# Kernel tuning notes

Measured on AMD Instinct MI355X. Metric: run time of the kernel, lower is better.

The kernel has to match this reference:

```python
import jax, jax.numpy as jnp
import numpy as np

DIM = 2048
H = 16
DK = 128
DV = 128
KCONV = 4
EPS = 1e-6
B = 2
S = 2048
KD = H * DK  # 2048
VD = H * DV  # 2048


def setup_inputs() -> dict:
    key = jax.random.key(0)
    ks = jax.random.split(key, 16)
    sc = 0.02
    inp = {
        "x": jax.random.normal(ks[0], (B, S, DIM), dtype=jnp.float32),
        "Wq": jax.random.normal(ks[1], (KD, DIM), dtype=jnp.float32) * sc,
        "Wk": jax.random.normal(ks[2], (KD, DIM), dtype=jnp.float32) * sc,
        "Wv": jax.random.normal(ks[3], (VD, DIM), dtype=jnp.float32) * sc,
        "Wa": jax.random.normal(ks[4], (H, DIM), dtype=jnp.float32) * sc,
        "Wb": jax.random.normal(ks[5], (H, DIM), dtype=jnp.float32) * sc,
        "Wg": jax.random.normal(ks[6], (VD, DIM), dtype=jnp.float32) * sc,
        "Wo": jax.random.normal(ks[7], (DIM, VD), dtype=jnp.float32) * sc,
        "cw_q": jax.random.normal(ks[8], (KD, KCONV), dtype=jnp.float32) * 0.3,
        "cb_q": jnp.zeros((KD,), dtype=jnp.float32),
        "cw_k": jax.random.normal(ks[9], (KD, KCONV), dtype=jnp.float32) * 0.3,
        "cb_k": jnp.zeros((KD,), dtype=jnp.float32),
        "cw_v": jax.random.normal(ks[10], (VD, KCONV), dtype=jnp.float32) * 0.3,
        "cb_v": jnp.zeros((VD,), dtype=jnp.float32),
        "A_log": jnp.zeros((H,), dtype=jnp.float32),
        "dt_bias": jnp.zeros((H,), dtype=jnp.float32),
        "norm_w": jnp.ones((VD,), dtype=jnp.float32),
    }
    return inp


def _causal_conv(x, w, b):
    # x: [B, S, C]; w: [C, K]; b: [C]. Depthwise causal conv (zero init state) + SiLU.
    Bb, Ss, C = x.shape
    xp = jnp.pad(x, ((0, 0), (KCONV - 1, 0), (0, 0)))
    out = b
    for j in range(KCONV):
        out = out + xp[:, j:j + Ss, :] * w[:, j]
    return jax.nn.silu(out)


def _l2norm(x):
    n = jnp.sqrt(jnp.sum(x * x, axis=-1, keepdims=True))
    return x / jnp.maximum(n, 1e-12)


def _forward(x, Wq, Wk, Wv, Wa, Wb, Wg, Wo, cw_q, cb_q, cw_k, cb_k, cw_v, cb_v,
             A_log, dt_bias, norm_w):
    Bb, Ss, _ = x.shape
    q = _causal_conv(x @ Wq.T, cw_q, cb_q)  # [B,S,KD]
    k = _causal_conv(x @ Wk.T, cw_k, cb_k)
    v = _causal_conv(x @ Wv.T, cw_v, cb_v)

    a = x @ Wa.T  # [B,S,H]
    b = x @ Wb.T
    g = jnp.exp(-jnp.exp(A_log)[None, None, :] * jax.nn.softplus(a + dt_bias[None, None, :]))
    beta = jax.nn.sigmoid(b)

    q = _l2norm(q.reshape(Bb, Ss, H, DK))
    k = _l2norm(k.reshape(Bb, Ss, H, DK))
    v = v.reshape(Bb, Ss, H, DV)

    S0 = jnp.zeros((Bb, H, DK, DV), dtype=x.dtype)

    def step(Sstate, inputs):
        q_t, k_t, v_t, g_t, beta_t = inputs  # [B,H,DK],[B,H,DK],[B,H,DV],[B,H],[B,H]
        retrieved = jnp.einsum('bhkv,bhk->bhv', Sstate, k_t)
        error = v_t - g_t[..., None] * retrieved
        update = k_t[..., :, None] * (beta_t[..., None] * error)[..., None, :]
        Snew = g_t[..., None, None] * Sstate + update
        o_t = jnp.einsum('bhkv,bhk->bhv', Snew, q_t)
        return Snew, o_t

    # scan over time: move time axis to front
    xs = (q.transpose(1, 0, 2, 3), k.transpose(1, 0, 2, 3), v.transpose(1, 0, 2, 3),
          g.transpose(1, 0, 2), beta.transpose(1, 0, 2))
    _, o = jax.lax.scan(step, S0, xs)  # o: [S,B,H,DV]
    o = o.transpose(1, 0, 2, 3).reshape(Bb, Ss, VD)

    # RMSNorm
    o = o * jax.lax.rsqrt(jnp.mean(o * o, axis=-1, keepdims=True) + EPS) * norm_w
    o = o * jax.nn.silu(x @ Wg.T)
    return o @ Wo.T


def reference(x, Wq, Wk, Wv, Wa, Wb, Wg, Wo, cw_q, cb_q, cw_k, cb_k, cw_v, cb_v,
              A_log, dt_bias, norm_w):
    return _forward(x, Wq, Wk, Wv, Wa, Wb, Wg, Wo, cw_q, cb_q, cw_k, cb_k,
                    cw_v, cb_v, A_log, dt_bias, norm_w)
```

## Files before the change

kernel.cpp:

```cpp
#include <hip/hip_runtime.h>

#define S_LEN   2048
#define NH      16
#define DIM     2048
#define KD      2048
#define VD      2048
#define MB      1048576ull
#define CT      64
#define NC      32

typedef short  short8  __attribute__((ext_vector_type(8)));
typedef short  short4v __attribute__((ext_vector_type(4)));
typedef float  floatx4 __attribute__((ext_vector_type(4)));

#define MFMA(a, b, c) __builtin_amdgcn_mfma_f32_16x16x32_bf16((a), (b), (c), 0, 0, 0)

__device__ inline short f2bf(float x) {
    unsigned u = __float_as_uint(x);
    unsigned r = (u + 0x7fffu + ((u >> 16) & 1u)) >> 16;
    return (short)r;
}
__device__ inline float bf2f(short s) {
    return __uint_as_float(((unsigned)(unsigned short)s) << 16);
}
__device__ inline float silu_f(float x) { return x / (1.f + __expf(-x)); }

__device__ inline short8 neg8(short8 a) {
    unsigned* p = (unsigned*)&a;
    p[0] ^= 0x80008000u; p[1] ^= 0x80008000u;
    p[2] ^= 0x80008000u; p[3] ^= 0x80008000u;
    return a;
}

__device__ inline void load_lds16(const void* g, void* l) {
    __builtin_amdgcn_global_load_lds(
        (const __attribute__((address_space(1))) unsigned int*)g,
        (__attribute__((address_space(3))) unsigned int*)l, 16, 0, 0);
}

__global__ __launch_bounds__(256) void cvt_all_kernel(
    const float* __restrict__ x,  const float* __restrict__ Wq,
    const float* __restrict__ Wk, const float* __restrict__ Wv,
    const float* __restrict__ Wg, const float* __restrict__ Wo,
    short* __restrict__ xb,  short* __restrict__ Wqb, short* __restrict__ Wkb,
    short* __restrict__ Wvb, short* __restrict__ Wgb, short* __restrict__ Wob) {
    const float* in; short* out; int n8;
    switch (blockIdx.y) {
        case 0:  in = x;  out = xb;  n8 = 1048576; break;
        case 1:  in = Wq; out = Wqb; n8 = 524288;  break;
        case 2:  in = Wk; out = Wkb; n8 = 524288;  break;
        case 3:  in = Wv; out = Wvb; n8 = 524288;  break;
        case 4:  in = Wg; out = Wgb; n8 = 524288;  break;
        default: in = Wo; out = Wob; n8 = 524288;  break;
    }
    int i = blockIdx.x * 256 + threadIdx.x;
    if (i >= n8) return;
    float4 a = ((const float4*)in)[2 * i];
    float4 b = ((const float4*)in)[2 * i + 1];
    short8 o;
    o[0] = f2bf(a.x); o[1] = f2bf(a.y); o[2] = f2bf(a.z); o[3] = f2bf(a.w);
    o[4] = f2bf(b.x); o[5] = f2bf(b.y); o[6] = f2bf(b.z); o[7] = f2bf(b.w);
    ((short8*)out)[i] = o;
}

__device__ inline void store_c(float* C, size_t idx, float v) { C[idx] = v; }
__device__ inline void store_c(short* C, size_t idx, float v) { C[idx] = f2bf(v); }

template <typename OutT>
__device__ inline void gemm_tile(const short* __restrict__ A, const short* __restrict__ Bw,
                                 OutT* __restrict__ C, int mtile, int ntile) {
    __shared__ short lA[128 * 32];
    __shared__ short lB[128 * 32];
    const int K = 2048, N = 2048;
    int t    = threadIdx.x;
    int wave = t >> 6;
    int lane = t & 63;
    int m0 = mtile * 128, n0 = ntile * 128;
    int wm = (wave & 1) * 64;
    int wn = (wave >> 1) * 64;

    floatx4 acc[4][4];
#pragma unroll
    for (int i = 0; i < 4; ++i)
#pragma unroll
        for (int j = 0; j < 4; ++j) acc[i][j] = (floatx4){0.f, 0.f, 0.f, 0.f};

    int fr = lane & 15;
    int fk = (lane >> 4) * 8;

    for (int k0 = 0; k0 < K; k0 += 32) {
#pragma unroll
        for (int p = 0; p < 2; ++p) {
            int c   = p * 256 + t;
            int row = c >> 2, kp = c & 3;
            const short* ga = A  + (size_t)(m0 + row) * K + k0 + kp * 8;
            const short* gb = Bw + (size_t)(n0 + row) * K + k0 + kp * 8;
            short* la = lA + (size_t)(p * 256 + wave * 64) * 8;
            short* lb = lB + (size_t)(p * 256 + wave * 64) * 8;
            load_lds16(ga, la);
            load_lds16(gb, lb);
        }
        __syncthreads();
        short8 af[4], bfr[4];
#pragma unroll
        for (int i = 0; i < 4; ++i) af[i]  = *(const short8*)(lA + (wm + i * 16 + fr) * 32 + fk);
#pragma unroll
        for (int j = 0; j < 4; ++j) bfr[j] = *(const short8*)(lB + (wn + j * 16 + fr) * 32 + fk);
#pragma unroll
        for (int i = 0; i < 4; ++i)
#pragma unroll
            for (int j = 0; j < 4; ++j)
                acc[i][j] = MFMA(af[i], bfr[j], acc[i][j]);
        __syncthreads();
    }
    int cr = (lane >> 4) * 4;
    int cc = lane & 15;
#pragma unroll
    for (int i = 0; i < 4; ++i)
#pragma unroll
        for (int j = 0; j < 4; ++j)
#pragma unroll
            for (int r = 0; r < 4; ++r)
                store_c(C, (size_t)(m0 + wm + i * 16 + cr + r) * N + (n0 + wn + j * 16 + cc),
                        acc[i][j][r]);
}

__global__ __launch_bounds__(256) void gemm_qkvg(const short* __restrict__ A,
    const short* __restrict__ B0, const short* __restrict__ B1,
    const short* __restrict__ B2, const short* __restrict__ B3,
    short* __restrict__ C0, short* __restrict__ C1,
    short* __restrict__ C2, short* __restrict__ C3) {
    const short* Bw; short* C;
    switch (blockIdx.z) {
        case 0:  Bw = B0; C = C0; break;
        case 1:  Bw = B1; C = C1; break;
        case 2:  Bw = B2; C = C2; break;
        default: Bw = B3; C = C3; break;
    }
    gemm_tile<short>(A, Bw, C, blockIdx.x, blockIdx.y);
}

__global__ __launch_bounds__(256) void gemm_out(const short* __restrict__ A,
    const short* __restrict__ Bw, float* __restrict__ C) {
    gemm_tile<float>(A, Bw, C, blockIdx.x, blockIdx.y);
}

__global__ __launch_bounds__(256) void ab_kernel(const float* __restrict__ x,
    const float* __restrict__ Wa, const float* __restrict__ Wb,
    const float* __restrict__ Alog, const float* __restrict__ dtb,
    float* __restrict__ gdec, float* __restrict__ beta) {
    __shared__ float xs[2048];
    __shared__ float red[32][9];
    int m = blockIdx.x, t = threadIdx.x;
    const float* xr = x + (size_t)m * DIM;
    for (int i = t; i < 512; i += 256) ((float4*)xs)[i] = ((const float4*)xr)[i];
    __syncthreads();
    int col = t >> 3, part = t & 7;
    const float* wr = (col < 16) ? (Wa + (size_t)col * DIM) : (Wb + (size_t)(col - 16) * DIM);
    float s = 0.f;
    int kb = part * 256;
#pragma unroll 4
    for (int k = 0; k < 256; k += 4) {
        float4 xv = *(const float4*)(xs + kb + k);
        float4 wv = *(const float4*)(wr + kb + k);
        s += xv.x * wv.x + xv.y * wv.y + xv.z * wv.z + xv.w * wv.w;
    }
    red[col][part] = s;
    __syncthreads();
    if (t < 32) {
        float a = 0.f;
#pragma unroll
        for (int p = 0; p < 8; ++p) a += red[t][p];
        if (t < 16) {
            float sp = a + dtb[t];
            float softp = (sp > 20.f) ? sp : log1pf(expf(sp));
            gdec[(size_t)m * NH + t] = expf(-expf(Alog[t]) * softp);
        } else {
            int h = t - 16;
            beta[(size_t)m * NH + h] = 1.f / (1.f + expf(-a));
        }
    }
}

__global__ __launch_bounds__(256) void conv_kernel(
    const short* __restrict__ qr, const short* __restrict__ kr, const short* __restrict__ vr,
    const float* __restrict__ cwq, const float* __restrict__ cbq,
    const float* __restrict__ cwk, const float* __restrict__ cbk,
    const float* __restrict__ cwv, const float* __restrict__ cbv,
    short* __restrict__ qn, short* __restrict__ kn, short* __restrict__ vc) {
    int gw   = blockIdx.x * 4 + (threadIdx.x >> 6);
    int lane = threadIdx.x & 63;
    int h  = gw & (NH - 1);
    int m  = gw >> 4;
    int tt = m & (S_LEN - 1);
    int c  = h * 128 + lane * 2;
    size_t rowbase = (size_t)m * KD + c;

    float4 wq0 = ((const float4*)cwq)[c], wq1 = ((const float4*)cwq)[c + 1];
    float4 wk0 = ((const float4*)cwk)[c], wk1 = ((const float4*)cwk)[c + 1];
    float4 wv0 = ((const float4*)cwv)[c], wv1 = ((const float4*)cwv)[c + 1];
    float q0 = cbq[c], q1 = cbq[c + 1];
    float k0 = cbk[c], k1 = cbk[c + 1];
    float v0 = cbv[c], v1 = cbv[c + 1];
    const float* wq0a = (const float*)&wq0; const float* wq1a = (const float*)&wq1;
    const float* wk0a = (const float*)&wk0; const float* wk1a = (const float*)&wk1;
    const float* wv0a = (const float*)&wv0; const float* wv1a = (const float*)&wv1;
#pragma unroll
    for (int j = 0; j < 4; ++j) {
        int ts = tt - 3 + j;
        if (ts >= 0) {
            long long rb = (long long)rowbase + (long long)(j - 3) * KD;
            unsigned uq = *(const unsigned*)(qr + rb);
            unsigned uk = *(const unsigned*)(kr + rb);
            unsigned uv = *(const unsigned*)(vr + rb);
            q0 += bf2f((short)(uq & 0xffff)) * wq0a[j]; q1 += bf2f((short)(uq >> 16)) * wq1a[j];
            k0 += bf2f((short)(uk & 0xffff)) * wk0a[j]; k1 += bf2f((short)(uk >> 16)) * wk1a[j];
            v0 += bf2f((short)(uv & 0xffff)) * wv0a[j]; v1 += bf2f((short)(uv >> 16)) * wv1a[j];
        }
    }
    q0 = silu_f(q0); q1 = silu_f(q1);
    k0 = silu_f(k0); k1 = silu_f(k1);
    v0 = silu_f(v0); v1 = silu_f(v1);

    float sq = q0 * q0 + q1 * q1;
    float sk = k0 * k0 + k1 * k1;
#pragma unroll
    for (int off = 1; off < 64; off <<= 1) {
        sq += __shfl_xor(sq, off);
        sk += __shfl_xor(sk, off);
    }
    float iq = 1.f / fmaxf(sqrtf(sq), 1e-12f);
    float ik = 1.f / fmaxf(sqrtf(sk), 1e-12f);
    unsigned oq = (unsigned)(unsigned short)f2bf(q0 * iq) | ((unsigned)(unsigned short)f2bf(q1 * iq) << 16);
    unsigned ok = (unsigned)(unsigned short)f2bf(k0 * ik) | ((unsigned)(unsigned short)f2bf(k1 * ik) << 16);
    unsigned ov = (unsigned)(unsigned short)f2bf(v0)      | ((unsigned)(unsigned short)f2bf(v1)      << 16);
    *(unsigned*)(qn + rowbase) = oq;
    *(unsigned*)(kn + rowbase) = ok;
    *(unsigned*)(vc + rowbase) = ov;
}

__global__ __launch_bounds__(256) void solve_kernel(
    const short* __restrict__ kn, const short* __restrict__ vn,
    const float* __restrict__ gdec, const float* __restrict__ beta,
    short* __restrict__ UvT, short* __restrict__ Tk) {
    __shared__ short Pn[64][72];
    __shared__ short Pt[64][72];
    __shared__ short UT[128][72];
    __shared__ float Ls[64];
    __shared__ float Bs[64];

    int wg   = blockIdx.x;
    int half = wg & 1;
    int c    = (wg >> 1) & 31;
    int bh   = wg >> 6;
    int b = bh >> 4, h = bh & 15;
    int tid = threadIdx.x;
    int wave = tid >> 6, lane = tid & 63;
    int quad = lane >> 4, l16 = lane & 15;

    const short* Kb = kn + ((size_t)(b * S_LEN + c * CT)) * KD + h * 128;
    const short* Vb = vn + ((size_t)(b * S_LEN + c * CT)) * KD + h * 128;

    if (wave == 0) {
        float lg = __logf(gdec[((size_t)(b * S_LEN + c * CT) + lane) * NH + h]);
#pragma unroll
        for (int off = 1; off < 64; off <<= 1) {
            float y = __shfl_up(lg, off);
            if (lane >= off) lg += y;
        }
        Ls[lane] = lg;
        Bs[lane] = beta[((size_t)(b * S_LEN + c * CT) + lane) * NH + h];
    }
    __syncthreads();

    {
        floatx4 acc[4];
#pragma unroll
        for (int i = 0; i < 4; ++i) acc[i] = (floatx4){0.f, 0.f, 0.f, 0.f};
        for (int ks = 0; ks < 4; ++ks) {
            short8 af = *(const short8*)(Kb + (size_t)(wave * 16 + l16) * KD + ks * 32 + quad * 8);
#pragma unroll
            for (int it = 0; it < 4; ++it) {
                short8 bf = *(const short8*)(Kb + (size_t)(it * 16 + l16) * KD + ks * 32 + quad * 8);
                acc[it] = MFMA(af, bf, acc[it]);
            }
        }
#pragma unroll
        for (int it = 0; it < 4; ++it) {
            int icol = it * 16 + l16;
#pragma unroll
            for (int r = 0; r < 4; ++r) {
                int trow = wave * 16 + quad * 4 + r;
                float v = 0.f;
                if (icol < trow) v = -Bs[trow] * __expf(Ls[trow] - Ls[icol]) * acc[it][r];
                short bv = f2bf(v);
                Pn[trow][icol] = bv;
                Pt[icol][trow] = bv;
            }
        }
    }

    {
        const short* src = half ? Kb : Vb;
        int tr = tid >> 2, seg = (tid & 3) * 32;
        float s = Bs[tr] * (half ? __expf(Ls[tr]) : 1.f);
#pragma unroll
        for (int j = 0; j < 4; ++j) {
            short8 d = *(const short8*)(src + (size_t)tr * KD + seg + j * 8);
#pragma unroll
            for (int e = 0; e < 8; ++e)
                UT[seg + j * 8 + e][tr] = f2bf(bf2f(d[e]) * s);
        }
    }
    __syncthreads();

    for (int iter = 0; iter < 6; ++iter) {
        floatx4 acc[8];
#pragma unroll
        for (int nt = 0; nt < 8; ++nt) {
            short4v u4 = *(const short4v*)&UT[nt * 16 + l16][wave * 16 + quad * 4];
            floatx4 a;
#pragma unroll
            for (int e = 0; e < 4; ++e) a[e] = bf2f(u4[e]);
            acc[nt] = a;
        }
        for (int ks = 0; ks < 2; ++ks) {
            short8 af = *(const short8*)&Pn[wave * 16 + l16][ks * 32 + quad * 8];
#pragma unroll
            for (int nt = 0; nt < 8; ++nt) {
                short8 bf = *(const short8*)&UT[nt * 16 + l16][ks * 32 + quad * 8];
                acc[nt] = MFMA(af, bf, acc[nt]);
            }
        }
        __syncthreads();
        if (iter < 5) {
#pragma unroll
            for (int nt = 0; nt < 8; ++nt) {
                short4v w4;
#pragma unroll
                for (int e = 0; e < 4; ++e) w4[e] = f2bf(acc[nt][e]);
                *(short4v*)&UT[nt * 16 + l16][wave * 16 + quad * 4] = w4;
            }
            floatx4 pacc[4];
#pragma unroll
            for (int it = 0; it < 4; ++it) pacc[it] = (floatx4){0.f, 0.f, 0.f, 0.f};
            for (int ks = 0; ks < 2; ++ks) {
                short8 paf = *(const short8*)&Pn[wave * 16 + l16][ks * 32 + quad * 8];
#pragma unroll
                for (int it = 0; it < 4; ++it) {
                    short8 pbf = *(const short8*)&Pt[it * 16 + l16][ks * 32 + quad * 8];
                    pacc[it] = MFMA(paf, pbf, pacc[it]);
                }
            }
            __syncthreads();
#pragma unroll
            for (int it = 0; it < 4; ++it) {
                int icol = it * 16 + l16;
#pragma unroll
                for (int r = 0; r < 4; ++r) {
                    int trow = wave * 16 + quad * 4 + r;
                    short bv = f2bf(pacc[it][r]);
                    Pn[trow][icol] = bv;
                    Pt[icol][trow] = bv;
                }
            }
            __syncthreads();
        } else {
            size_t cb = (size_t)(bh * NC + c);
            if (half == 0) {
#pragma unroll
                for (int nt = 0; nt < 8; ++nt) {
                    short4v w4;
#pragma unroll
                    for (int e = 0; e < 4; ++e) w4[e] = f2bf(acc[nt][e]);
                    *(short4v*)(UvT + (cb * 128 + nt * 16 + l16) * 64 + wave * 16 + quad * 4) = w4;
                }
            } else {
#pragma unroll
                for (int nt = 0; nt < 8; ++nt)
#pragma unroll
                    for (int r = 0; r < 4; ++r)
                        Tk[(cb * 64 + wave * 16 + quad * 4 + r) * 128 + nt * 16 + l16] = f2bf(acc[nt][r]);
            }
        }
    }
}

__global__ __launch_bounds__(256) void prepb_kernel(
    const short* __restrict__ qn, const short* __restrict__ kn,
    const float* __restrict__ gdec,
    short* __restrict__ Wb_, short* __restrict__ Qg,
    short* __restrict__ KtT, float* __restrict__ gam63) {
    __shared__ short KT[128][72];
    __shared__ float Ls[64];
    int wg = blockIdx.x;
    int c = wg & 31, bh = wg >> 5;
    int b = bh >> 4, h = bh & 15;
    int tid = threadIdx.x, wave = tid >> 6, lane = tid & 63;
    int quad = lane >> 4, l16 = lane & 15;
    const short* Qb = qn + ((size_t)(b * S_LEN + c * CT)) * KD + h * 128;
    const short* Kb = kn + ((size_t)(b * S_LEN + c * CT)) * KD + h * 128;

    if (wave == 0) {
        float lg = __logf(gdec[((size_t)(b * S_LEN + c * CT) + lane) * NH + h]);
#pragma unroll
        for (int off = 1; off < 64; off <<= 1) {
            float y = __shfl_up(lg, off);
            if (lane >= off) lg += y;
        }
        Ls[lane] = lg;
    }
    __syncthreads();
    size_t cb = (size_t)(bh * NC + c);
    if (tid == 0) gam63[cb] = __expf(Ls[63]);

    {
        floatx4 acc[4];
#pragma unroll
        for (int i = 0; i < 4; ++i) acc[i] = (floatx4){0.f, 0.f, 0.f, 0.f};
        for (int ks = 0; ks < 4; ++ks) {
            short8 af = *(const short8*)(Qb + (size_t)(wave * 16 + l16) * KD + ks * 32 + quad * 8);
#pragma unroll
            for (int it = 0; it < 4; ++it) {
                short8 bf = *(const short8*)(Kb + (size_t)(it * 16 + l16) * KD + ks * 32 + quad * 8);
                acc[it] = MFMA(af, bf, acc[it]);
            }
        }
#pragma unroll
        for (int it = 0; it < 4; ++it) {
            int icol = it * 16 + l16;
#pragma unroll
            for (int r = 0; r < 4; ++r) {
                int trow = wave * 16 + quad * 4 + r;
                float v = (icol <= trow) ? __expf(Ls[trow] - Ls[icol]) * acc[it][r] : 0.f;
                Wb_[(cb * 64 + trow) * 64 + icol] = f2bf(v);
            }
        }
    }

    {
        int tr = tid >> 2, seg = (tid & 3) * 32;
        float sq = __expf(Ls[tr]);
        float sk = __expf(Ls[63] - Ls[tr]);
#pragma unroll
        for (int j = 0; j < 4; ++j) {
            short8 dq = *(const short8*)(Qb + (size_t)tr * KD + seg + j * 8);
            short8 dk = *(const short8*)(Kb + (size_t)tr * KD + seg + j * 8);
            short8 oq;
#pragma unroll
            for (int e = 0; e < 8; ++e) {
                oq[e] = f2bf(bf2f(dq[e]) * sq);
                KT[seg + j * 8 + e][tr] = f2bf(bf2f(dk[e]) * sk);
            }
            *(short8*)(Qg + (cb * 64 + tr) * 128 + seg + j * 8) = oq;
        }
    }
    __syncthreads();
    {
        int dk = tid >> 1, seg = (tid & 1) * 32;
#pragma unroll
        for (int j = 0; j < 4; ++j) {
            short8 v = *(const short8*)&KT[dk][seg + j * 8];
            *(short8*)(KtT + (cb * 128 + dk) * 64 + seg + j * 8) = v;
        }
    }
}

__global__ __launch_bounds__(256, 1) void seq_kernel(
    const short* __restrict__ UvT, const short* __restrict__ Tk,
    const short* __restrict__ Wb_, const short* __restrict__ Qg,
    const short* __restrict__ KtT, const float* __restrict__ gam63,
    short* __restrict__ ob) {
    __shared__ short ST[64][136];
    __shared__ short UTs[64][72];
    int wg = blockIdx.x;
    int vh = wg & 1, bh = wg >> 1;
    int b = bh >> 4, h = bh & 15;
    int tid = threadIdx.x, wave = tid >> 6, lane = tid & 63;
    int quad = lane >> 4, l16 = lane & 15;

    for (int i = tid; i < 64 * 136; i += 256) ((short*)ST)[i] = 0;
    floatx4 sacc[8];
#pragma unroll
    for (int i = 0; i < 8; ++i) sacc[i] = (floatx4){0.f, 0.f, 0.f, 0.f};
    __syncthreads();

    short8 tkA[4], qgA[4], wA[2], ktA[16]; short4v uvA[4]; float gamA;
    short8 tkB[4], qgB[4], wB[2], ktB[16]; short4v uvB[4]; float gamB;

#define LOADF(tkX, qgX, wX, ktX, uvX, gamX, c)                                              \
    {                                                                                       \
        size_t cb = (size_t)(bh * NC + (c));                                                \
        const short* Tkc = Tk  + cb * 64 * 128;                                             \
        const short* Qgc = Qg  + cb * 64 * 128;                                             \
        const short* Wc  = Wb_ + cb * 64 * 64;                                              \
        const short* Ktc = KtT + cb * 128 * 64;                                             \
        const short* Uvc = UvT + (cb * 128 + (size_t)vh * 64) * 64;                         \
        _Pragma("unroll")                                                                   \
        for (int ks = 0; ks < 4; ++ks) {                                                    \
            tkX[ks] = *(const short8*)(Tkc + (size_t)(wave * 16 + l16) * 128 + ks * 32 + quad * 8); \
            qgX[ks] = *(const short8*)(Qgc + (size_t)(wave * 16 + l16) * 128 + ks * 32 + quad * 8); \
        }                                                                                   \
        _Pragma("unroll")                                                                   \
        for (int ks = 0; ks < 2; ++ks)                                                      \
            wX[ks] = *(const short8*)(Wc + (size_t)(wave * 16 + l16) * 64 + ks * 32 + quad * 8); \
        _Pragma("unroll")                                                                   \
        for (int dt = 0; dt < 8; ++dt)                                                      \
            _Pragma("unroll")                                                               \
            for (int ks = 0; ks < 2; ++ks)                                                  \
                ktX[dt * 2 + ks] = *(const short8*)(Ktc + (size_t)(dt * 16 + l16) * 64 + ks * 32 + quad * 8); \
        _Pragma("unroll")                                                                   \
        for (int vt = 0; vt < 4; ++vt)                                                      \
            uvX[vt] = *(const short4v*)(Uvc + (size_t)(vt * 16 + l16) * 64 + wave * 16 + quad * 4); \
        gamX = gam63[cb];                                                                   \
    }

#define BODY(tkX, qgX, wX, ktX, uvX, gamX, c)                                               \
    {                                                                                       \
        floatx4 uacc[4], oacc[4];                                                           \
        _Pragma("unroll")                                                                   \
        for (int vt = 0; vt < 4; ++vt) {                                                    \
            floatx4 a;                                                                      \
            _Pragma("unroll")                                                               \
            for (int e = 0; e < 4; ++e) a[e] = bf2f(uvX[vt][e]);                            \
            uacc[vt] = a;                                                                   \
            oacc[vt] = (floatx4){0.f, 0.f, 0.f, 0.f};                                       \
        }                                                                                   \
        _Pragma("unroll")                                                                   \
        for (int ks = 0; ks < 4; ++ks) {                                                    \
            short8 afT = neg8(tkX[ks]);                                                     \
            _Pragma("unroll")                                                               \
            for (int vt = 0; vt < 4; ++vt) {                                                \
                short8 bf = *(const short8*)&ST[vt * 16 + l16][ks * 32 + quad * 8];         \
                uacc[vt] = MFMA(afT, bf, uacc[vt]);                                         \
                oacc[vt] = MFMA(qgX[ks], bf, oacc[vt]);                                     \
            }                                                                               \
        }                                                                                   \
        _Pragma("unroll")                                                                   \
        for (int vt = 0; vt < 4; ++vt) {                                                    \
            short4v w4;                                                                     \
            _Pragma("unroll")                                                               \
            for (int e = 0; e < 4; ++e) w4[e] = f2bf(uacc[vt][e]);                          \
            *(short4v*)&UTs[vt * 16 + l16][wave * 16 + quad * 4] = w4;                      \
        }                                                                                   \
        __syncthreads();                                                                    \
        _Pragma("unroll")                                                                   \
        for (int ks = 0; ks < 2; ++ks) {                                                    \
            _Pragma("unroll")                                                               \
            for (int vt = 0; vt < 4; ++vt) {                                                \
                short8 bf = *(const short8*)&UTs[vt * 16 + l16][ks * 32 + quad * 8];        \
                oacc[vt] = MFMA(wX[ks], bf, oacc[vt]);                                      \
            }                                                                               \
        }                                                                                   \
        _Pragma("unroll")                                                                   \
        for (int vt = 0; vt < 4; ++vt)                                                      \
            _Pragma("unroll")                                                               \
            for (int r = 0; r < 4; ++r) {                                                   \
                int m = b * S_LEN + (c) * CT + wave * 16 + quad * 4 + r;                    \
                ob[(size_t)m * VD + h * 128 + vh * 64 + vt * 16 + l16] = f2bf(oacc[vt][r]); \
            }                                                                               \
        _Pragma("unroll")                                                                   \
        for (int dt = 0; dt < 8; ++dt)                                                      \
            _Pragma("unroll")                                                               \
            for (int e = 0; e < 4; ++e) sacc[dt][e] *= gamX;                                \
        _Pragma("unroll")                                                                   \
        for (int ks = 0; ks < 2; ++ks) {                                                    \
            short8 af = *(const short8*)&UTs[wave * 16 + l16][ks * 32 + quad * 8];          \
            _Pragma("unroll")                                                               \
            for (int dt = 0; dt < 8; ++dt)                                                  \
                sacc[dt] = MFMA(af, ktX[dt * 2 + ks], sacc[dt]);                            \
        }                                                                                   \
        _Pragma("unroll")                                                                   \
        for (int dt = 0; dt < 8; ++dt)                                                      \
            _Pragma("unroll")                                                               \
            for (int r = 0; r < 4; ++r)                                                     \
                ST[wave * 16 + quad * 4 + r][dt * 16 + l16] = f2bf(sacc[dt][r]);            \
        __syncthreads();                                                                    \
    }

    LOADF(tkA, qgA, wA, ktA, uvA, gamA, 0)
    for (int c = 0; c < NC; c += 2) {
        LOADF(tkB, qgB, wB, ktB, uvB, gamB, c + 1)
        BODY(tkA, qgA, wA, ktA, uvA, gamA, c)
        if (c + 2 < NC) LOADF(tkA, qgA, wA, ktA, uvA, gamA, c + 2)
        BODY(tkB, qgB, wB, ktB, uvB, gamB, c + 1)
    }
#undef LOADF
#undef BODY
}

__global__ __launch_bounds__(256) void rms_gate_kernel(
    const short* __restrict__ o, const short* __restrict__ graw,
    const float* __restrict__ nw, short* __restrict__ og) {
    __shared__ float red[4];
    int m = blockIdx.x, t = threadIdx.x;
    short8 a = ((const short8*)(o + (size_t)m * VD))[t];
    float av[8];
#pragma unroll
    for (int i = 0; i < 8; ++i) av[i] = bf2f(a[i]);
    float ss = 0.f;
#pragma unroll
    for (int i = 0; i < 8; ++i) ss += av[i] * av[i];
#pragma unroll
    for (int off = 1; off < 64; off <<= 1) ss += __shfl_xor(ss, off);
    if ((t & 63) == 0) red[t >> 6] = ss;
    __syncthreads();
    float tot = red[0] + red[1] + red[2] + red[3];
    float sc = rsqrtf(tot * (1.f / VD) + 1e-6f);
    short8 gv = ((const short8*)(graw + (size_t)m * VD))[t];
    float4 n0 = ((const float4*)nw)[2 * t];
    float4 n1 = ((const float4*)nw)[2 * t + 1];
    const float* na = (const float*)&n0;
    const float* nb = (const float*)&n1;
    short8 ov;
#pragma unroll
    for (int i = 0; i < 4; ++i) ov[i]     = f2bf(av[i]     * sc * na[i] * silu_f(bf2f(gv[i])));
#pragma unroll
    for (int i = 0; i < 4; ++i) ov[i + 4] = f2bf(av[i + 4] * sc * nb[i] * silu_f(bf2f(gv[i + 4])));
    ((short8*)(og + (size_t)m * VD))[t] = ov;
}

extern "C" void kernel_launch(void* const* d_in, const int* in_sizes, int n_in,
                              void* d_out, int out_size, void* d_ws, size_t ws_size,
                              hipStream_t stream) {
    const float* x    = (const float*)d_in[0];
    const float* Wq   = (const float*)d_in[1];
    const float* Wk   = (const float*)d_in[2];
    const float* Wv   = (const float*)d_in[3];
    const float* Wa   = (const float*)d_in[4];
    const float* Wb   = (const float*)d_in[5];
    const float* Wg   = (const float*)d_in[6];
    const float* Wo   = (const float*)d_in[7];
    const float* cwq  = (const float*)d_in[8];
    const float* cbq  = (const float*)d_in[9];
    const float* cwk  = (const float*)d_in[10];
    const float* cbk  = (const float*)d_in[11];
    const float* cwv  = (const float*)d_in[12];
    const float* cbv  = (const float*)d_in[13];
    const float* Alog = (const float*)d_in[14];
    const float* dtb  = (const float*)d_in[15];
    const float* nw   = (const float*)d_in[16];

    char* ws = (char*)d_ws;
    short* Wob = (short*)(ws);
    short* xb  = (short*)(ws + 8 * MB);
    short* Wqb = (short*)(ws + 24 * MB);
    short* Wkb = (short*)(ws + 32 * MB);
    short* Wvb = (short*)(ws + 40 * MB);
    short* Wgb = (short*)(ws + 48 * MB);
    short* qrb = (short*)(ws + 56 * MB);
    short* krb = (short*)(ws + 72 * MB);
    short* vrb = (short*)(ws + 88 * MB);
    short* grb = (short*)(ws + 104 * MB);
    short* qnb = (short*)(ws + 8 * MB);
    short* knb = (short*)(ws + 24 * MB);
    short* vnb = (short*)(ws + 40 * MB);
    float* gdec = (float*)(ws + 120 * MB);
    float* beta = (float*)(ws + 120 * MB + 262144);
    short* ob  = qrb;
    short* ogb = krb;
    short* UvT  = (short*)(ws + 121 * MB);
    short* Tkb  = (short*)(ws + 137 * MB);
    short* Wbuf = (short*)(ws + 153 * MB);
    short* Qgb  = (short*)(ws + 161 * MB);
    short* KtT  = (short*)(ws + 177 * MB);
    float* gm63 = (float*)(ws + 193 * MB);

    cvt_all_kernel<<<dim3(4096, 6), 256, 0, stream>>>(x, Wq, Wk, Wv, Wg, Wo,
                                                      xb, Wqb, Wkb, Wvb, Wgb, Wob);

    ab_kernel<<<4096, 256, 0, stream>>>(x, Wa, Wb, Alog, dtb, gdec, beta);

    gemm_qkvg<<<dim3(32, 16, 4), 256, 0, stream>>>(xb, Wqb, Wkb, Wvb, Wgb,
                                                   qrb, krb, vrb, grb);

    conv_kernel<<<16384, 256, 0, stream>>>(qrb, krb, vrb,
                                           cwq, cbq, cwk, cbk, cwv, cbv, qnb, knb, vnb);

    solve_kernel<<<2048, 256, 0, stream>>>(knb, vnb, gdec, beta, UvT, Tkb);
    prepb_kernel<<<1024, 256, 0, stream>>>(qnb, knb, gdec, Wbuf, Qgb, KtT, gm63);
    seq_kernel<<<64, 256, 0, stream>>>(UvT, Tkb, Wbuf, Qgb, KtT, gm63, ob);

    rms_gate_kernel<<<4096, 256, 0, stream>>>(ob, grb, nw, ogb);

    gemm_out<<<dim3(32, 16, 1), 256, 0, stream>>>(ogb, Wob, (float*)d_out);
}
```

Baseline: 783.4 us.

## Replace QKVG GEMM with 256x256-tile 8-wave kernel using 4-stage LDS pipeline

The fused Q/K/V/G projection GEMM now uses a new kernel with 256x256 output tiles, 512 threads and a 4-deep ring of LDS stages filled by asynchronous global-to-LDS loads. Loads run three k-steps ahead and are paced with explicit vmcnt waits and barriers, with XOR swizzling to avoid LDS bank conflicts. Block indices are remapped to group tiles for L2 locality, and s_setprio is raised around MFMA bursts. The larger tile raises reuse per loaded byte, but it needs 128KB of dynamic shared memory, so only one block fits per CU, and the hand-placed wait counts are fragile if anything about the loads changes.

```diff
diff --git a/kernel.cpp b/kernel.cpp
--- a/kernel.cpp
+++ b/kernel.cpp
@@ -125,11 +125,65 @@
                         acc[i][j][r]);
 }
 
-__global__ __launch_bounds__(256) void gemm_qkvg(const short* __restrict__ A,
+__global__ __launch_bounds__(256) void gemm_out(const short* __restrict__ A,
+    const short* __restrict__ Bw, float* __restrict__ C) {
+    gemm_tile<float>(A, Bw, C, blockIdx.x, blockIdx.y);
+}
+
+
+#define VM(n_) asm volatile("s_waitcnt vmcnt(" #n_ ")" ::: "memory");
+
+#define STAGE8(s_, isB_)                                                     \
+    {                                                                        \
+        const char* gsrc = (isB_) ? (const char*)Bw : (const char*)A;        \
+        int t0 = (isB_) ? n0 : m0;                                           \
+        char* dbase = smem + ((s_) & 3) * 32768 + (isB_) * 16384;            \
+        _Pragma("unroll")                                                    \
+        for (int ld = 0; ld < 2; ++ld) {                                     \
+            int ch = ld * 8 + wave;                                          \
+            int Pl = (ch << 10) + (lane << 4);                               \
+            int Q  = Pl ^ (((lane >> 2) & 3) << 4);                          \
+            const char* src = gsrc + ((size_t)(t0 + (Q >> 6)) << 12)         \
+                              + ((size_t)(s_) << 6) + (Q & 63);              \
+            load_lds16(src, dbase + (ch << 10));                             \
+        }                                                                    \
+    }
+
+#define PHASE8(s_, qm_, LOADB_, STG, WAIT)                                   \
+    {                                                                        \
+        const char* sb = smem + ((s_) & 3) * 32768;                          \
+        short8 af[4];                                                        \
+        if (LOADB_) {                                                        \
+            _Pragma("unroll")                                                \
+            for (int nf = 0; nf < 4; ++nf)                                   \
+                bfr[nf] = *(const short8*)(sb + 16384 +                      \
+                    ((rowB_base + nf * 16) << 6) + qsw);                     \
+        }                                                                    \
+        _Pragma("unroll")                                                    \
+        for (int mf = 0; mf < 4; ++mf)                                       \
+            af[mf] = *(const short8*)(sb +                                   \
+                ((rowA_base + (qm_) * 64 + mf * 16) << 6) + qsw);            \
+        STG                                                                  \
+        __builtin_amdgcn_s_barrier();                                        \
+        asm volatile("s_waitcnt lgkmcnt(0)" ::: "memory");                   \
+        __builtin_amdgcn_s_setprio(1);                                       \
+        _Pragma("unroll")                                                    \
+        for (int mf = 0; mf < 4; ++mf)                                       \
+            _Pragma("unroll")                                                \
+            for (int nf = 0; nf < 4; ++nf)                                   \
+                acc[(qm_) * 4 + mf][nf] =                                    \
+                    MFMA(af[mf], bfr[nf], acc[(qm_) * 4 + mf][nf]);          \
+        __builtin_amdgcn_s_setprio(0);                                       \
+        WAIT                                                                 \
+        __builtin_amdgcn_s_barrier();                                        \
+    }
+
+__global__ __launch_bounds__(512) void gemm8_qkvg(const short* __restrict__ A,
     const short* __restrict__ B0, const short* __restrict__ B1,
     const short* __restrict__ B2, const short* __restrict__ B3,
     short* __restrict__ C0, short* __restrict__ C1,
     short* __restrict__ C2, short* __restrict__ C3) {
+    extern __shared__ char smem[];
     const short* Bw; short* C;
     switch (blockIdx.z) {
         case 0:  Bw = B0; C = C0; break;
@@ -137,12 +191,59 @@
         case 2:  Bw = B2; C = C2; break;
         default: Bw = B3; C = C3; break;
     }
-    gemm_tile<short>(A, Bw, C, blockIdx.x, blockIdx.y);
-}
-
-__global__ __launch_bounds__(256) void gemm_out(const short* __restrict__ A,
-    const short* __restrict__ Bw, float* __restrict__ C) {
-    gemm_tile<float>(A, Bw, C, blockIdx.x, blockIdx.y);
+    int x  = blockIdx.x;
+    int xs = (x & 7) * 16 + (x >> 3);
+    int m0 = (xs >> 3) * 256;
+    int n0 = (xs & 7) * 256;
+    int tid  = threadIdx.x;
+    int wave = tid >> 6, lane = tid & 63;
+    int l16  = lane & 15, quad = lane >> 4;
+    int wm = wave >> 2, wn = wave & 3;
+    int qsw = ((quad ^ (l16 & 3)) << 4);
+    int rowA_base = wm * 128 + l16;
+    int rowB_base = wn * 64 + l16;
+
+    floatx4 acc[8][4];
+#pragma unroll
+    for (int i = 0; i < 8; ++i)
+#pragma unroll
+        for (int j = 0; j < 4; ++j) acc[i][j] = (floatx4){0.f, 0.f, 0.f, 0.f};
+    short8 bfr[4];
+
+    STAGE8(0, 0) STAGE8(0, 1)
+    STAGE8(1, 0) STAGE8(1, 1)
+    STAGE8(2, 0) STAGE8(2, 1)
+    VM(8)
+    __builtin_amdgcn_s_barrier();
+
+#pragma unroll 1
+    for (int T = 0; T < 30; ++T) {
+        int s0 = 2 * T, s1 = 2 * T + 1, sa = 2 * T + 3, sb2 = 2 * T + 4;
+        PHASE8(s0, 0, 1, STAGE8(sa, 0), )
+        PHASE8(s0, 1, 0, STAGE8(sa, 1), VM(8))
+        PHASE8(s1, 0, 1, STAGE8(sb2, 0), )
+        PHASE8(s1, 1, 0, STAGE8(sb2, 1), VM(8))
+    }
+    PHASE8(60, 0, 1, STAGE8(63, 0), )
+    PHASE8(60, 1, 0, STAGE8(63, 1), VM(8))
+    PHASE8(61, 0, 1, , )
+    PHASE8(61, 1, 0, , VM(4))
+    PHASE8(62, 0, 1, , )
+    PHASE8(62, 1, 0, , VM(0))
+    PHASE8(63, 0, 1, , )
+    PHASE8(63, 1, 0, , )
+
+#pragma unroll
+    for (int i = 0; i < 8; ++i) {
+        int row0 = m0 + wm * 128 + (i >> 2) * 64 + (i & 3) * 16 + quad * 4;
+#pragma unroll
+        for (int nf = 0; nf < 4; ++nf) {
+            int col = n0 + wn * 64 + nf * 16 + l16;
+#pragma unroll
+            for (int r = 0; r < 4; ++r)
+                C[(size_t)(row0 + r) * 2048 + col] = f2bf(acc[i][nf][r]);
+        }
+    }
 }
 
 __global__ __launch_bounds__(256) void ab_kernel(const float* __restrict__ x,
@@ -666,13 +767,20 @@
     short* KtT  = (short*)(ws + 177 * MB);
     float* gm63 = (float*)(ws + 193 * MB);
 
+    static bool attr_done = false;
+    if (!attr_done) {
+        hipFuncSetAttribute((const void*)gemm8_qkvg,
+                            hipFuncAttributeMaxDynamicSharedMemorySize, 131072);
+        attr_done = true;
+    }
+
     cvt_all_kernel<<<dim3(4096, 6), 256, 0, stream>>>(x, Wq, Wk, Wv, Wg, Wo,
                                                       xb, Wqb, Wkb, Wvb, Wgb, Wob);
 
     ab_kernel<<<4096, 256, 0, stream>>>(x, Wa, Wb, Alog, dtb, gdec, beta);
 
-    gemm_qkvg<<<dim3(32, 16, 4), 256, 0, stream>>>(xb, Wqb, Wkb, Wvb, Wgb,
-                                                   qrb, krb, vrb, grb);
+    gemm8_qkvg<<<dim3(128, 1, 4), 512, 131072, stream>>>(xb, Wqb, Wkb, Wvb, Wgb,
+                                                         qrb, krb, vrb, grb);
 
     conv_kernel<<<16384, 256, 0, stream>>>(qrb, krb, vrb,
                                            cwq, cbq, cwk, cbk, cwv, cbv, qnb, knb, vnb);
```

Result: no change. 775.2 us (-1.0%).
